# Kernel tuning notes

Measured on AMD Instinct MI355X. Metric: run time of the kernel, lower is better.

The kernel has to match this reference:

```python
import jax, jax.numpy as jnp
import numpy as np

V, K, M_FWD, M_BWD = 100000, 64, 16, 16
SIGMA = 1.0

def _alpha_init(key, m_half, k):
    # banded init: -10 everywhere, 0 on a strided band, + 0.1*randn
    a = np.full((m_half, k), -10.0, dtype=np.float32)
    stride = max(1, k // m_half)
    for i in range(m_half):
        a[i, i * stride: min(i * stride + stride, k)] = 0.0
    return jnp.asarray(a) + 0.1 * jax.random.normal(key, (m_half, k), dtype=jnp.float32)

def setup_inputs() -> dict:
    key = jax.random.key(0)
    k1, k2, k3, k4 = jax.random.split(key, 4)
    return {
        "d_out_t": jax.random.normal(k1, (V, K), dtype=jnp.float32),
        "d_in_t": jax.random.normal(k2, (V, K), dtype=jnp.float32),
        "alpha_fwd": _alpha_init(k3, M_FWD, K),
        "alpha_bwd": _alpha_init(k4, M_BWD, K),
    }

def _compress(phi, alpha, sigma):
    # phi: (V, K); alpha: (m_half, K) -> z: (V, m_half, K)
    z = phi[:, None, :] + alpha[None, :, :]
    return sigma * jax.scipy.special.logsumexp(z / sigma, axis=-1)

def reference(d_out_t, d_in_t, alpha_fwd, alpha_bwd):
    y_fwd = _compress(d_out_t, alpha_fwd, SIGMA)  # (V, m_fwd)
    y_bwd = _compress(d_in_t, alpha_bwd, SIGMA)   # (V, m_bwd)
    return (y_fwd, y_bwd)
```

## Files before the change

kernel.cpp:

```cpp
#include <hip/hip_runtime.h>


#define K_DIM 64

__global__ __launch_bounds__(256) void prep_ealpha_kernel(
    const float* __restrict__ alpha_fwd,
    const float* __restrict__ alpha_bwd,
    float* __restrict__ ea)
{
    int i = blockIdx.x * 256 + threadIdx.x;
    float a = (i < 1024) ? alpha_fwd[i] : alpha_bwd[i - 1024];
    ea[i] = __expf(a);
}

__global__ __launch_bounds__(256) void dual_compress_kernel(
    const float* __restrict__ d_out_t,
    const float* __restrict__ d_in_t,
    const float* __restrict__ ea,
    float* __restrict__ out, int V)
{
    int tid  = threadIdx.x;
    int lane = tid & 63;
    int w    = tid >> 6;
    int c    = w & 1;
    int rh   = w >> 1;
    int v    = blockIdx.x * 128 + rh * 64 + lane;
    int vc   = (v < V) ? v : (V - 1);

    const float* base = c ? d_in_t : d_out_t;
    const float4* p = (const float4*)(base + (size_t)vc * K_DIM);

    float4 e4[16];
    #pragma unroll
    for (int i = 0; i < 16; ++i) {
        float4 q = p[i];
        e4[i].x = __expf(q.x); e4[i].y = __expf(q.y);
        e4[i].z = __expf(q.z); e4[i].w = __expf(q.w);
    }

    const float* eac = ea + __builtin_amdgcn_readfirstlane(c << 10);

    float acc[16];
    #pragma unroll
    for (int mi = 0; mi < 16; ++mi) acc[mi] = 0.0f;

    #pragma unroll
    for (int kc = 0; kc < 16; ++kc) {
        float4 e = e4[kc];
        #pragma unroll
        for (int mi = 0; mi < 16; ++mi) {
            const float* arow = eac + mi * K_DIM + kc * 4;
            acc[mi] = fmaf(e.x, arow[0], acc[mi]);
            acc[mi] = fmaf(e.y, arow[1], acc[mi]);
            acc[mi] = fmaf(e.z, arow[2], acc[mi]);
            acc[mi] = fmaf(e.w, arow[3], acc[mi]);
        }
    }

    if (v < V) {
        float* orow = out + ((size_t)c * V + v) * 16;
        #pragma unroll
        for (int i = 0; i < 4; ++i) {
            float4 y;
            y.x = __logf(acc[4*i+0]);
            y.y = __logf(acc[4*i+1]);
            y.z = __logf(acc[4*i+2]);
            y.w = __logf(acc[4*i+3]);
            ((float4*)orow)[i] = y;
        }
    }
}

extern "C" void kernel_launch(void* const* d_in, const int* in_sizes, int n_in,
                              void* d_out, int out_size, void* d_ws, size_t ws_size,
                              hipStream_t stream) {
    const float* d_out_t   = (const float*)d_in[0];
    const float* d_in_t    = (const float*)d_in[1];
    const float* alpha_fwd = (const float*)d_in[2];
    const float* alpha_bwd = (const float*)d_in[3];
    float* out = (float*)d_out;
    float* ea  = (float*)d_ws;

    int V = in_sizes[0] / K_DIM;

    prep_ealpha_kernel<<<8, 256, 0, stream>>>(alpha_fwd, alpha_bwd, ea);

    int grid = (V + 127) / 128;
    dual_compress_kernel<<<grid, 256, 0, stream>>>(
        d_out_t, d_in_t, ea, out, V);
}
```

Before: 101.5 us.

## Stage input rows through padded LDS for coalesced global loads

Before, each lane read its own 256-byte row with strided float4 loads. Now each wave loads a contiguous 64-row tile with fully coalesced float4 loads, transposes it through a padded shared-memory buffer, and then has each lane read its row back from LDS. The block shrinks to 128 threads covering 64 rows per tensor. This adds LDS traffic and about 33 KB of shared memory per block, which may limit occupancy. The LDS writes, all in the wave's own private slice, are read back with no barrier.

```diff
diff --git a/kernel.cpp b/kernel.cpp
--- a/kernel.cpp
+++ b/kernel.cpp
@@ -2,6 +2,7 @@
 
 
 #define K_DIM 64
+#define PAD   65
 
 __global__ __launch_bounds__(256) void prep_ealpha_kernel(
     const float* __restrict__ alpha_fwd,
@@ -13,30 +14,38 @@
     ea[i] = __expf(a);
 }
 
-__global__ __launch_bounds__(256) void dual_compress_kernel(
+__global__ __launch_bounds__(128) void dual_compress_kernel(
     const float* __restrict__ d_out_t,
     const float* __restrict__ d_in_t,
     const float* __restrict__ ea,
     float* __restrict__ out, int V)
 {
+    __shared__ float stage[2][64 * PAD];
+
     int tid  = threadIdx.x;
     int lane = tid & 63;
     int w    = tid >> 6;
-    int c    = w & 1;
-    int rh   = w >> 1;
-    int v    = blockIdx.x * 128 + rh * 64 + lane;
-    int vc   = (v < V) ? v : (V - 1);
+    int c    = w;
+    int wavebase = blockIdx.x * 64;
+    const float* base = c ? d_in_t : d_out_t;
 
-    const float* base = c ? d_in_t : d_out_t;
-    const float4* p = (const float4*)(base + (size_t)vc * K_DIM);
+    float* st = stage[w];
+    size_t maxoff = (size_t)V * K_DIM - 4;
+    #pragma unroll
+    for (int j = 0; j < 16; ++j) {
+        size_t eoff = (size_t)wavebase * K_DIM + (size_t)j * 256 + (size_t)lane * 4;
+        if (eoff > maxoff) eoff = maxoff;
+        float4 q = *(const float4*)(base + eoff);
+        int row = j * 4 + (lane >> 4);
+        int col = (lane & 15) * 4;
+        float* d = st + row * PAD + col;
+        d[0] = q.x; d[1] = q.y; d[2] = q.z; d[3] = q.w;
+    }
 
-    float4 e4[16];
+    const float* my = st + lane * PAD;
+    float e[64];
     #pragma unroll
-    for (int i = 0; i < 16; ++i) {
-        float4 q = p[i];
-        e4[i].x = __expf(q.x); e4[i].y = __expf(q.y);
-        e4[i].z = __expf(q.z); e4[i].w = __expf(q.w);
-    }
+    for (int k = 0; k < 64; ++k) e[k] = __expf(my[k]);
 
     const float* eac = ea + __builtin_amdgcn_readfirstlane(c << 10);
 
@@ -46,17 +55,17 @@
 
     #pragma unroll
     for (int kc = 0; kc < 16; ++kc) {
-        float4 e = e4[kc];
         #pragma unroll
         for (int mi = 0; mi < 16; ++mi) {
             const float* arow = eac + mi * K_DIM + kc * 4;
-            acc[mi] = fmaf(e.x, arow[0], acc[mi]);
-            acc[mi] = fmaf(e.y, arow[1], acc[mi]);
-            acc[mi] = fmaf(e.z, arow[2], acc[mi]);
-            acc[mi] = fmaf(e.w, arow[3], acc[mi]);
+            acc[mi] = fmaf(e[kc*4+0], arow[0], acc[mi]);
+            acc[mi] = fmaf(e[kc*4+1], arow[1], acc[mi]);
+            acc[mi] = fmaf(e[kc*4+2], arow[2], acc[mi]);
+            acc[mi] = fmaf(e[kc*4+3], arow[3], acc[mi]);
         }
     }
 
+    int v = wavebase + lane;
     if (v < V) {
         float* orow = out + ((size_t)c * V + v) * 16;
         #pragma unroll
@@ -85,7 +94,7 @@
 
     prep_ealpha_kernel<<<8, 256, 0, stream>>>(alpha_fwd, alpha_bwd, ea);
 
-    int grid = (V + 127) / 128;
-    dual_compress_kernel<<<grid, 256, 0, stream>>>(
+    int grid = (V + 63) / 64;
+    dual_compress_kernel<<<grid, 128, 0, stream>>>(
         d_out_t, d_in_t, ea, out, V);
 }
```

Measured after the change: 107.6 us. +6.0%, slower.
